# Performance work log

Hardware: AMD Instinct MI355X
Metric: run time of the kernel (lower is better)

Reference implementation:

```python
import jax, jax.numpy as jnp
import numpy as np

N = 100000      # nodes
E = 1200000     # edges (avg degree 12)
IN, H, OUT = 128, 64, 47
NUM_CONVS = 4   # num_layers=3 hidden SAGEConvs + 1 output SAGEConv


def setup_inputs() -> dict:
    key = jax.random.key(0)
    ks = jax.random.split(key, 2 + 1 + 2 * NUM_CONVS)
    x = jax.random.normal(ks[0], (N, IN), dtype=jnp.float32)
    edge_index = jax.random.randint(ks[1], (2, E), 0, N, dtype=jnp.int32)

    def lin(k, out_d, in_d):
        return jax.random.normal(k, (out_d, in_d), dtype=jnp.float32) / np.float32(np.sqrt(in_d))

    inp = {"x": x, "edge_index": edge_index}
    inp["W_in"] = lin(ks[2], H, IN)
    inp["b_in"] = jnp.zeros((H,), jnp.float32)
    dims = [(H, H), (H, H), (H, H), (OUT, H)]
    for i, (o, d) in enumerate(dims):
        inp[f"Wl{i}"] = lin(ks[3 + 2 * i], o, d)   # lin_l: applied to mean-aggregated neighbors (has bias)
        inp[f"Wr{i}"] = lin(ks[4 + 2 * i], o, d)   # lin_r: applied to root/self features (no bias)
        inp[f"bl{i}"] = jnp.zeros((o,), jnp.float32)
    return inp


def _sage_conv(x, src, dst, deg_inv, Wl, bl, Wr):
    # PyG SAGEConv (mean aggr): out_i = Wl @ mean_{j->i} x_j + bl + Wr @ x_i
    msg = x[src]                                               # [E, d] gather
    agg = jax.ops.segment_sum(msg, dst, num_segments=N)        # [N, d] scatter-add
    agg = agg * deg_inv[:, None]                               # mean
    return agg @ Wl.T + bl + x @ Wr.T


def reference(x, edge_index, W_in, b_in,
              Wl0, Wr0, bl0, Wl1, Wr1, bl1, Wl2, Wr2, bl2, Wl3, Wr3, bl3):
    src, dst = edge_index[0], edge_index[1]
    deg = jax.ops.segment_sum(jnp.ones((E,), x.dtype), dst, num_segments=N)
    deg_inv = jnp.where(deg > 0, 1.0 / jnp.maximum(deg, 1.0), 0.0)

    x = x @ W_in.T + b_in                                      # inProj
    inp = x
    x = jax.nn.relu(x)

    layers = [(Wl0, bl0, Wr0), (Wl1, bl1, Wr1), (Wl2, bl2, Wr2), (Wl3, bl3, Wr3)]
    for i, (Wl, bl, Wr) in enumerate(layers):
        x = _sage_conv(x, src, dst, deg_inv, Wl, bl, Wr)
        if i != NUM_CONVS - 1:
            x = jax.nn.relu(x)
            # dropout is identity in eval mode (training=False)
            x = x + 0.2 * inp
    return jax.nn.log_softmax(x, axis=-1)
```

## Files before the change

### kernel.cpp

```cpp
#include <hip/hip_runtime.h>
#include <hip/hip_fp16.h>

#define NN 100000
#define NE 1200000
#define DIN 128
#define DH 64
#define DOUT_FINAL 47
#define NPB 4
#define NBKT 391
#define EB 4096

typedef _Float16 half8 __attribute__((ext_vector_type(8)));
typedef float floatx4 __attribute__((ext_vector_type(4)));


__global__ void bucket_hist_k(const int* __restrict__ dst, int* __restrict__ bktCnt) {
    __shared__ int h[NBKT];
    int tid = threadIdx.x;
    for (int i = tid; i < NBKT; i += 256) h[i] = 0;
    __syncthreads();
    for (int e = blockIdx.x * 256 + tid; e < NE; e += gridDim.x * 256)
        atomicAdd(&h[dst[e] >> 8], 1);
    __syncthreads();
    for (int i = tid; i < NBKT; i += 256)
        if (h[i]) atomicAdd(&bktCnt[i], h[i]);
}

__global__ void bscan_k(const int* __restrict__ bktCnt, int* __restrict__ bktPtr) {
    __shared__ int s[512];
    int tid = threadIdx.x;
    int v = (tid < NBKT) ? bktCnt[tid] : 0;
    s[tid] = v;
    __syncthreads();
    for (int off = 1; off < 512; off <<= 1) {
        int t = (tid >= off) ? s[tid - off] : 0;
        __syncthreads();
        s[tid] += t;
        __syncthreads();
    }
    if (tid < NBKT) bktPtr[tid] = s[tid] - v;
    if (tid == 0) bktPtr[NBKT] = NE;
}

__global__ void scatter_pairs_k(const int* __restrict__ src, const int* __restrict__ dst,
                                const int* __restrict__ bktPtr, int* __restrict__ bktCur,
                                int2* __restrict__ pairs) {
    __shared__ int h[NBKT];
    __shared__ int base[NBKT];
    __shared__ int cur[NBKT];
    int tid = threadIdx.x;
    int e0 = blockIdx.x * EB;
    int e1 = e0 + EB < NE ? e0 + EB : NE;
    for (int i = tid; i < NBKT; i += 256) { h[i] = 0; cur[i] = 0; }
    __syncthreads();
    for (int e = e0 + tid; e < e1; e += 256)
        atomicAdd(&h[dst[e] >> 8], 1);
    __syncthreads();
    for (int i = tid; i < NBKT; i += 256) {
        int c = h[i];
        base[i] = bktPtr[i] + (c ? atomicAdd(&bktCur[i], c) : 0);
    }
    __syncthreads();
    for (int e = e0 + tid; e < e1; e += 256) {
        int d = dst[e];
        int b = d >> 8;
        int p = base[b] + atomicAdd(&cur[b], 1);
        pairs[p] = make_int2(src[e], d);
    }
}

__global__ void count_node_k(const int2* __restrict__ pairs, const int* __restrict__ bktPtr,
                             int* __restrict__ cnt) {
    __shared__ int h[256];
    int tid = threadIdx.x;
    int b = blockIdx.x;
    h[tid] = 0;
    __syncthreads();
    int e1 = bktPtr[b + 1];
    for (int e = bktPtr[b] + tid; e < e1; e += 256)
        atomicAdd(&h[pairs[e].y & 255], 1);
    __syncthreads();
    int node = (b << 8) + tid;
    if (node < NN) cnt[node] = h[tid];
}

__global__ void scan1_k(const int* __restrict__ cnt, int* __restrict__ ptr,
                        int* __restrict__ bsum, float* __restrict__ dinv) {
    __shared__ int s[256];
    int tid = threadIdx.x;
    int i = blockIdx.x * 256 + tid;
    int v = (i < NN) ? cnt[i] : 0;
    s[tid] = v;
    __syncthreads();
    for (int off = 1; off < 256; off <<= 1) {
        int t = (tid >= off) ? s[tid - off] : 0;
        __syncthreads();
        s[tid] += t;
        __syncthreads();
    }
    if (i < NN) {
        ptr[i] = s[tid] - v;
        dinv[i] = (v > 0) ? 1.0f / (float)v : 0.0f;
    }
    if (tid == 255) bsum[blockIdx.x] = s[255];
}

__global__ void scan2_k(int* __restrict__ bsum, int nb) {
    __shared__ int s[512];
    int tid = threadIdx.x;
    int v = (tid < nb) ? bsum[tid] : 0;
    s[tid] = v;
    __syncthreads();
    for (int off = 1; off < 512; off <<= 1) {
        int t = (tid >= off) ? s[tid - off] : 0;
        __syncthreads();
        s[tid] += t;
        __syncthreads();
    }
    if (tid < nb) bsum[tid] = s[tid] - v;
}

__global__ void scan3_k(int* __restrict__ ptr, const int* __restrict__ bsum) {
    int i = blockIdx.x * 256 + threadIdx.x;
    if (i < NN) ptr[i] += bsum[blockIdx.x];
    if (i == 0) ptr[NN] = NE;
}

__global__ void fill_bucket_k(const int2* __restrict__ pairs, const int* __restrict__ bktPtr,
                              const int* __restrict__ ptr, int* __restrict__ csrc) {
    __shared__ int cur[256];
    __shared__ int sptr[256];
    int tid = threadIdx.x;
    int b = blockIdx.x;
    cur[tid] = 0;
    int node = (b << 8) + tid;
    sptr[tid] = (node < NN) ? ptr[node] : 0;
    __syncthreads();
    int e1 = bktPtr[b + 1];
    for (int e = bktPtr[b] + tid; e < e1; e += 256) {
        int2 pr = pairs[e];
        int lo = pr.y & 255;
        int r = atomicAdd(&cur[lo], 1);
        csrc[sptr[lo] + r] = pr.x;
    }
}


__global__ void convert_x_k(const float* __restrict__ x, __half* __restrict__ xh) {
    int i = (blockIdx.x * 256 + threadIdx.x) * 8;
    if (i >= NN * DIN) return;
    float4 v0 = *(const float4*)&x[i];
    float4 v1 = *(const float4*)&x[i + 4];
    union { __half h[8]; uint4 u; } pk;
    pk.h[0] = __float2half(v0.x); pk.h[1] = __float2half(v0.y);
    pk.h[2] = __float2half(v0.z); pk.h[3] = __float2half(v0.w);
    pk.h[4] = __float2half(v1.x); pk.h[5] = __float2half(v1.y);
    pk.h[6] = __float2half(v1.z); pk.h[7] = __float2half(v1.w);
    *(uint4*)&xh[i] = pk.u;
}

__global__ void convert_w_k(const float* __restrict__ Win,
                            const float* __restrict__ Wl0, const float* __restrict__ Wr0,
                            const float* __restrict__ Wl1, const float* __restrict__ Wr1,
                            const float* __restrict__ Wl2, const float* __restrict__ Wr2,
                            const float* __restrict__ Wl3, const float* __restrict__ Wr3,
                            __half* __restrict__ wh) {
    int id = blockIdx.x * 256 + threadIdx.x;
    if (id >= 8192 + 8 * 4096) return;
    float v;
    if (id < 8192) {
        v = Win[id];
    } else {
        int q = id - 8192;
        int mi = q >> 12;
        int local = q & 4095;
        int r = local >> 6, c = local & 63;
        const float* srcs[8] = {Wl0, Wr0, Wl1, Wr1, Wl2, Wr2, Wl3, Wr3};
        int dout = (mi >= 6) ? DOUT_FINAL : 64;
        v = (r < dout) ? srcs[mi][r * 64 + c] : 0.0f;
    }
    wh[id] = __float2half(v);
}


__global__ __launch_bounds__(256) void gemm_in_mfma(const _Float16* __restrict__ Xh,
                                                    const _Float16* __restrict__ Wh,
                                                    const float* __restrict__ bias,
                                                    __half* __restrict__ hinph,
                                                    __half* __restrict__ xah) {
    int wave = threadIdx.x >> 6, lane = threadIdx.x & 63;
    int lr = lane & 15, kg = lane >> 4;
    int m0 = blockIdx.x * 128 + wave * 32;
    floatx4 acc[2][4];
    #pragma unroll
    for (int mt = 0; mt < 2; ++mt)
        #pragma unroll
        for (int nt = 0; nt < 4; ++nt) acc[mt][nt] = (floatx4){0.f, 0.f, 0.f, 0.f};
    half8 az = {};
    #pragma unroll
    for (int kc = 0; kc < 4; ++kc) {
        half8 a[2];
        #pragma unroll
        for (int mt = 0; mt < 2; ++mt) {
            int m = m0 + mt * 16 + lr;
            a[mt] = (m < NN) ? *(const half8*)&Xh[(size_t)m * 128 + kc * 32 + kg * 8] : az;
        }
        #pragma unroll
        for (int nt = 0; nt < 4; ++nt) {
            half8 b = *(const half8*)&Wh[(size_t)(nt * 16 + lr) * 128 + kc * 32 + kg * 8];
            #pragma unroll
            for (int mt = 0; mt < 2; ++mt)
                acc[mt][nt] = __builtin_amdgcn_mfma_f32_16x16x32_f16(a[mt], b, acc[mt][nt], 0, 0, 0);
        }
    }
    #pragma unroll
    for (int mt = 0; mt < 2; ++mt)
        #pragma unroll
        for (int nt = 0; nt < 4; ++nt) {
            int n = nt * 16 + lr;
            float bv = bias[n];
            #pragma unroll
            for (int j = 0; j < 4; ++j) {
                int m = m0 + mt * 16 + kg * 4 + j;
                if (m < NN) {
                    float v = acc[mt][nt][j] + bv;
                    hinph[(size_t)m * 64 + n] = __float2half(v);
                    xah[(size_t)m * 64 + n] = __float2half(fmaxf(v, 0.0f));
                }
            }
        }
}

__global__ __launch_bounds__(256) void gemm_dual_mfma(const _Float16* __restrict__ Xh,
                                                      const _Float16* __restrict__ Wlh,
                                                      const _Float16* __restrict__ Wrh,
                                                      __half* __restrict__ ylh,
                                                      __half* __restrict__ yrh) {
    int wave = threadIdx.x >> 6, lane = threadIdx.x & 63;
    int lr = lane & 15, kg = lane >> 4;
    int m0 = blockIdx.x * 128 + wave * 32;
    floatx4 accL[2][4], accR[2][4];
    #pragma unroll
    for (int mt = 0; mt < 2; ++mt)
        #pragma unroll
        for (int nt = 0; nt < 4; ++nt) {
            accL[mt][nt] = (floatx4){0.f, 0.f, 0.f, 0.f};
            accR[mt][nt] = (floatx4){0.f, 0.f, 0.f, 0.f};
        }
    half8 az = {};
    #pragma unroll
    for (int kc = 0; kc < 2; ++kc) {
        half8 a[2];
        #pragma unroll
        for (int mt = 0; mt < 2; ++mt) {
            int m = m0 + mt * 16 + lr;
            a[mt] = (m < NN) ? *(const half8*)&Xh[(size_t)m * 64 + kc * 32 + kg * 8] : az;
        }
        #pragma unroll
        for (int nt = 0; nt < 4; ++nt) {
            half8 bl = *(const half8*)&Wlh[(size_t)(nt * 16 + lr) * 64 + kc * 32 + kg * 8];
            half8 br = *(const half8*)&Wrh[(size_t)(nt * 16 + lr) * 64 + kc * 32 + kg * 8];
            #pragma unroll
            for (int mt = 0; mt < 2; ++mt) {
                accL[mt][nt] = __builtin_amdgcn_mfma_f32_16x16x32_f16(a[mt], bl, accL[mt][nt], 0, 0, 0);
                accR[mt][nt] = __builtin_amdgcn_mfma_f32_16x16x32_f16(a[mt], br, accR[mt][nt], 0, 0, 0);
            }
        }
    }
    #pragma unroll
    for (int mt = 0; mt < 2; ++mt)
        #pragma unroll
        for (int nt = 0; nt < 4; ++nt) {
            int n = nt * 16 + lr;
            #pragma unroll
            for (int j = 0; j < 4; ++j) {
                int m = m0 + mt * 16 + kg * 4 + j;
                if (m < NN) {
                    ylh[(size_t)m * 64 + n] = __float2half(accL[mt][nt][j]);
                    yrh[(size_t)m * 64 + n] = __float2half(accR[mt][nt][j]);
                }
            }
        }
}


__device__ __forceinline__ float2 gather_sum2(const __half* __restrict__ ylh,
                                              const int* __restrict__ csrc,
                                              int eb, int ee, int lane) {
    int half = lane >> 5;
    int fo = (lane & 31) * 4;
    const char* base = (const char*)ylh;
    float accx = 0.0f, accy = 0.0f;
    for (int e0 = eb; e0 < ee; e0 += 64) {
        int rem = ee - e0;
        int m = rem < 64 ? rem : 64;
        int sv = (lane < m) ? csrc[e0 + lane] : 0;
        int j = 0;
        for (; j + 8 <= m; j += 8) {
            int sA = __shfl(sv, j + 0 + half);
            int sB = __shfl(sv, j + 2 + half);
            int sC = __shfl(sv, j + 4 + half);
            int sD = __shfl(sv, j + 6 + half);
            float2 a = __half22float2(*(const __half2*)(base + (sA * 128 + fo)));
            float2 b = __half22float2(*(const __half2*)(base + (sB * 128 + fo)));
            float2 c = __half22float2(*(const __half2*)(base + (sC * 128 + fo)));
            float2 d = __half22float2(*(const __half2*)(base + (sD * 128 + fo)));
            accx += (a.x + b.x) + (c.x + d.x);
            accy += (a.y + b.y) + (c.y + d.y);
        }
        for (; j + 2 <= m; j += 2) {
            int s = __shfl(sv, j + half);
            float2 a = __half22float2(*(const __half2*)(base + (s * 128 + fo)));
            accx += a.x;
            accy += a.y;
        }
        if (j < m) {
            int s = __shfl(sv, j);
            if (half == 0) {
                float2 a = __half22float2(*(const __half2*)(base + (s * 128 + fo)));
                accx += a.x;
                accy += a.y;
            }
        }
    }
    accx += __shfl_xor(accx, 32);
    accy += __shfl_xor(accy, 32);
    return make_float2(accx, accy);
}


__global__ void aggregate_mid_k(const __half* __restrict__ ylh, const __half* __restrict__ yrh,
                                const __half* __restrict__ hinph,
                                const int* __restrict__ ptr, const int* __restrict__ csrc,
                                const float* __restrict__ dinv, const float* __restrict__ bl,
                                __half* __restrict__ outp) {
    int tid = threadIdx.x;
    int w = tid >> 6, lane = tid & 63;
    int i = blockIdx.x * NPB + w;
    if (i >= NN) return;
    float2 acc = gather_sum2(ylh, csrc, ptr[i], ptr[i + 1], lane);
    int half = lane >> 5;
    int f0 = (lane & 31) * 2;
    float dv = dinv[i];
    float2 yrv = __half22float2(*(const __half2*)&yrh[(size_t)i * 64 + f0]);
    float2 blv = *(const float2*)&bl[f0];
    float2 hv = __half22float2(*(const __half2*)&hinph[(size_t)i * 64 + f0]);
    float rx = fmaxf(acc.x * dv + yrv.x + blv.x, 0.0f) + 0.2f * hv.x;
    float ry = fmaxf(acc.y * dv + yrv.y + blv.y, 0.0f) + 0.2f * hv.y;
    if (half == 0) {
        __half2 hv2;
        hv2.x = __float2half(rx);
        hv2.y = __float2half(ry);
        *(__half2*)&outp[(size_t)i * 64 + f0] = hv2;
    }
}


__global__ void aggregate_final_k(const __half* __restrict__ ylh, const __half* __restrict__ yrh,
                                  const int* __restrict__ ptr, const int* __restrict__ csrc,
                                  const float* __restrict__ dinv, const float* __restrict__ bl,
                                  float* __restrict__ outp) {
    int tid = threadIdx.x;
    int w = tid >> 6, lane = tid & 63;
    int i = blockIdx.x * NPB + w;
    if (i >= NN) return;
    float2 acc = gather_sum2(ylh, csrc, ptr[i], ptr[i + 1], lane);
    int half = lane >> 5;
    int f0 = (lane & 31) * 2;
    float dv = dinv[i];
    float2 yrv = __half22float2(*(const __half2*)&yrh[(size_t)i * 64 + f0]);
    float b0 = (f0 < DOUT_FINAL) ? bl[f0] : 0.0f;
    float b1 = (f0 + 1 < DOUT_FINAL) ? bl[f0 + 1] : 0.0f;
    float vx = (f0 < DOUT_FINAL) ? acc.x * dv + yrv.x + b0 : -__builtin_inff();
    float vy = (f0 + 1 < DOUT_FINAL) ? acc.y * dv + yrv.y + b1 : -__builtin_inff();
    float mx = fmaxf(vx, vy);
    for (int o = 16; o; o >>= 1) mx = fmaxf(mx, __shfl_xor(mx, o));
    float ex = ((f0 < DOUT_FINAL) ? expf(vx - mx) : 0.0f) +
               ((f0 + 1 < DOUT_FINAL) ? expf(vy - mx) : 0.0f);
    float s = ex;
    for (int o = 16; o; o >>= 1) s += __shfl_xor(s, o);
    float ls = logf(s);
    if (half == 0) {
        if (f0 < DOUT_FINAL)     outp[(size_t)i * DOUT_FINAL + f0] = vx - mx - ls;
        if (f0 + 1 < DOUT_FINAL) outp[(size_t)i * DOUT_FINAL + f0 + 1] = vy - mx - ls;
    }
}


extern "C" void kernel_launch(void* const* d_in, const int* in_sizes, int n_in,
                              void* d_out, int out_size, void* d_ws, size_t ws_size,
                              hipStream_t stream) {
    const float* x    = (const float*)d_in[0];
    const int*   ei   = (const int*)d_in[1];
    const float* Win  = (const float*)d_in[2];
    const float* bin  = (const float*)d_in[3];
    const float* Wl0  = (const float*)d_in[4];
    const float* Wr0  = (const float*)d_in[5];
    const float* bl0  = (const float*)d_in[6];
    const float* Wl1  = (const float*)d_in[7];
    const float* Wr1  = (const float*)d_in[8];
    const float* bl1  = (const float*)d_in[9];
    const float* Wl2  = (const float*)d_in[10];
    const float* Wr2  = (const float*)d_in[11];
    const float* bl2  = (const float*)d_in[12];
    const float* Wl3  = (const float*)d_in[13];
    const float* Wr3  = (const float*)d_in[14];
    const float* bl3  = (const float*)d_in[15];
    float* out = (float*)d_out;

    const int* src = ei;
    const int* dst = ei + NE;

    size_t off = 0;
    auto alloc = [&](size_t bytes) -> void* {
        void* p = (char*)d_ws + off;
        off += (bytes + 255) & ~(size_t)255;
        return p;
    };
    int*    bkt    = (int*)alloc((size_t)2 * NBKT * 4);
    int*    bktPtr = (int*)alloc((size_t)(NBKT + 1) * 4);
    int2*   pairs  = (int2*)alloc((size_t)NE * 8);
    int*    cnt    = (int*)alloc((size_t)NN * 4);
    int*    ptr    = (int*)alloc((size_t)(NN + 1) * 4);
    float*  dinv   = (float*)alloc((size_t)NN * 4);
    int*    csrc   = (int*)alloc((size_t)NE * 4);
    int*    bsum   = (int*)alloc(512 * 4);
    __half* xh     = (__half*)alloc((size_t)NN * 128 * 2);
    __half* wh     = (__half*)alloc((size_t)(8192 + 8 * 4096) * 2);
    __half* hinph  = (__half*)alloc((size_t)NN * 64 * 2);
    __half* xah    = (__half*)alloc((size_t)NN * 64 * 2);
    __half* xbh    = (__half*)alloc((size_t)NN * 64 * 2);
    __half* ylh    = (__half*)alloc((size_t)NN * 64 * 2);
    __half* yrh    = (__half*)alloc((size_t)NN * 64 * 2);
    int*    bktCnt = bkt;
    int*    bktCur = bkt + NBKT;

    __half* Winh = wh;
    __half* Wl0h = wh + 8192;
    __half* Wr0h = Wl0h + 4096;
    __half* Wl1h = Wr0h + 4096;
    __half* Wr1h = Wl1h + 4096;
    __half* Wl2h = Wr1h + 4096;
    __half* Wr2h = Wl2h + 4096;
    __half* Wl3h = Wr2h + 4096;
    __half* Wr3h = Wl3h + 4096;

    const int NB_NODE = (NN + 255) / 256;
    const int NB_AGG  = (NN + NPB - 1) / NPB;
    const int NB_GEMM = (NN + 127) / 128;
    const int NB_SCAT = (NE + EB - 1) / EB;
    const int NB_XC   = (NN * DIN / 8 + 255) / 256;
    const int NB_WC   = (8192 + 8 * 4096 + 255) / 256;

    convert_x_k<<<NB_XC, 256, 0, stream>>>(x, xh);
    convert_w_k<<<NB_WC, 256, 0, stream>>>(Win, Wl0, Wr0, Wl1, Wr1, Wl2, Wr2, Wl3, Wr3, wh);

    hipMemsetAsync(bkt, 0, (size_t)2 * NBKT * 4, stream);
    bucket_hist_k<<<512, 256, 0, stream>>>(dst, bktCnt);
    bscan_k<<<1, 512, 0, stream>>>(bktCnt, bktPtr);
    scatter_pairs_k<<<NB_SCAT, 256, 0, stream>>>(src, dst, bktPtr, bktCur, pairs);
    count_node_k<<<NBKT, 256, 0, stream>>>(pairs, bktPtr, cnt);
    scan1_k<<<NB_NODE, 256, 0, stream>>>(cnt, ptr, bsum, dinv);
    scan2_k<<<1, 512, 0, stream>>>(bsum, NB_NODE);
    scan3_k<<<NB_NODE, 256, 0, stream>>>(ptr, bsum);
    fill_bucket_k<<<NBKT, 256, 0, stream>>>(pairs, bktPtr, ptr, csrc);

    gemm_in_mfma<<<NB_GEMM, 256, 0, stream>>>((const _Float16*)xh, (const _Float16*)Winh, bin, hinph, xah);

    gemm_dual_mfma<<<NB_GEMM, 256, 0, stream>>>((const _Float16*)xah, (const _Float16*)Wl0h, (const _Float16*)Wr0h, ylh, yrh);
    aggregate_mid_k<<<NB_AGG, 256, 0, stream>>>(ylh, yrh, hinph, ptr, csrc, dinv, bl0, xbh);
    gemm_dual_mfma<<<NB_GEMM, 256, 0, stream>>>((const _Float16*)xbh, (const _Float16*)Wl1h, (const _Float16*)Wr1h, ylh, yrh);
    aggregate_mid_k<<<NB_AGG, 256, 0, stream>>>(ylh, yrh, hinph, ptr, csrc, dinv, bl1, xah);
    gemm_dual_mfma<<<NB_GEMM, 256, 0, stream>>>((const _Float16*)xah, (const _Float16*)Wl2h, (const _Float16*)Wr2h, ylh, yrh);
    aggregate_mid_k<<<NB_AGG, 256, 0, stream>>>(ylh, yrh, hinph, ptr, csrc, dinv, bl2, xbh);
    gemm_dual_mfma<<<NB_GEMM, 256, 0, stream>>>((const _Float16*)xbh, (const _Float16*)Wl3h, (const _Float16*)Wr3h, ylh, yrh);
    aggregate_final_k<<<NB_AGG, 256, 0, stream>>>(ylh, yrh, ptr, csrc, dinv, bl3, out);
}
```

Measured before the change: 343.7 us.

## Interleave gathers for four nodes per wavefront in aggregation kernels

Each wavefront now aggregates four destination nodes instead of one. The gather loops for the four nodes are interleaved so more independent memory loads are in flight per wave, which is meant to hide gather latency and cut per-wave setup overhead. Blocks now cover 16 nodes, so there are fewer blocks. The risks are load imbalance when the four degrees differ, extra control flow and register use, and lower occupancy.

```diff
diff --git a/kernel.cpp b/kernel.cpp
--- a/kernel.cpp
+++ b/kernel.cpp
@@ -6,7 +6,7 @@
 #define DIN 128
 #define DH 64
 #define DOUT_FINAL 47
-#define NPB 4
+#define NPB4 16
 #define NBKT 391
 #define EB 4096
 
@@ -284,48 +284,85 @@
 }
 
 
-__device__ __forceinline__ float2 gather_sum2(const __half* __restrict__ ylh,
-                                              const int* __restrict__ csrc,
-                                              int eb, int ee, int lane) {
+#define GQ_BODY8(sv, j, ax, ay)                                                   \
+    {                                                                             \
+        int sA = __shfl(sv, j + 0 + half);                                        \
+        int sB = __shfl(sv, j + 2 + half);                                        \
+        int sC = __shfl(sv, j + 4 + half);                                        \
+        int sD = __shfl(sv, j + 6 + half);                                        \
+        float2 a = __half22float2(*(const __half2*)(base + (sA * 128 + fo)));     \
+        float2 b = __half22float2(*(const __half2*)(base + (sB * 128 + fo)));     \
+        float2 c = __half22float2(*(const __half2*)(base + (sC * 128 + fo)));     \
+        float2 d = __half22float2(*(const __half2*)(base + (sD * 128 + fo)));     \
+        ax += (a.x + b.x) + (c.x + d.x);                                          \
+        ay += (a.y + b.y) + (c.y + d.y);                                          \
+    }
+#define GQ_BODY2(sv, j, ax, ay)                                                   \
+    {                                                                             \
+        int s = __shfl(sv, j + half);                                             \
+        float2 a = __half22float2(*(const __half2*)(base + (s * 128 + fo)));      \
+        ax += a.x; ay += a.y;                                                     \
+    }
+#define GQ_BODY1(sv, j, ax, ay)                                                   \
+    {                                                                             \
+        int s = __shfl(sv, j);                                                    \
+        if (half == 0) {                                                          \
+            float2 a = __half22float2(*(const __half2*)(base + (s * 128 + fo)));  \
+            ax += a.x; ay += a.y;                                                 \
+        }                                                                         \
+    }
+
+__device__ __forceinline__ void gather_quad(const __half* __restrict__ ylh,
+                                            const int* __restrict__ csrc,
+                                            int eb0, int ee0, int eb1, int ee1,
+                                            int eb2, int ee2, int eb3, int ee3,
+                                            int lane,
+                                            float2& r0, float2& r1, float2& r2, float2& r3) {
     int half = lane >> 5;
     int fo = (lane & 31) * 4;
     const char* base = (const char*)ylh;
-    float accx = 0.0f, accy = 0.0f;
-    for (int e0 = eb; e0 < ee; e0 += 64) {
-        int rem = ee - e0;
-        int m = rem < 64 ? rem : 64;
-        int sv = (lane < m) ? csrc[e0 + lane] : 0;
-        int j = 0;
-        for (; j + 8 <= m; j += 8) {
-            int sA = __shfl(sv, j + 0 + half);
-            int sB = __shfl(sv, j + 2 + half);
-            int sC = __shfl(sv, j + 4 + half);
-            int sD = __shfl(sv, j + 6 + half);
-            float2 a = __half22float2(*(const __half2*)(base + (sA * 128 + fo)));
-            float2 b = __half22float2(*(const __half2*)(base + (sB * 128 + fo)));
-            float2 c = __half22float2(*(const __half2*)(base + (sC * 128 + fo)));
-            float2 d = __half22float2(*(const __half2*)(base + (sD * 128 + fo)));
-            accx += (a.x + b.x) + (c.x + d.x);
-            accy += (a.y + b.y) + (c.y + d.y);
-        }
-        for (; j + 2 <= m; j += 2) {
-            int s = __shfl(sv, j + half);
-            float2 a = __half22float2(*(const __half2*)(base + (s * 128 + fo)));
-            accx += a.x;
-            accy += a.y;
-        }
-        if (j < m) {
-            int s = __shfl(sv, j);
-            if (half == 0) {
-                float2 a = __half22float2(*(const __half2*)(base + (s * 128 + fo)));
-                accx += a.x;
-                accy += a.y;
-            }
-        }
-    }
-    accx += __shfl_xor(accx, 32);
-    accy += __shfl_xor(accy, 32);
-    return make_float2(accx, accy);
+    float a0x = 0.f, a0y = 0.f, a1x = 0.f, a1y = 0.f;
+    float a2x = 0.f, a2y = 0.f, a3x = 0.f, a3y = 0.f;
+
+    int e0 = eb0, e1 = eb1, e2 = eb2, e3 = eb3;
+    while (e0 < ee0 || e1 < ee1 || e2 < ee2 || e3 < ee3) {
+        int m0 = 0, m1 = 0, m2 = 0, m3 = 0;
+        int sv0 = 0, sv1 = 0, sv2 = 0, sv3 = 0;
+        if (e0 < ee0) { int r = ee0 - e0; m0 = r < 64 ? r : 64; sv0 = (lane < m0) ? csrc[e0 + lane] : 0; }
+        if (e1 < ee1) { int r = ee1 - e1; m1 = r < 64 ? r : 64; sv1 = (lane < m1) ? csrc[e1 + lane] : 0; }
+        if (e2 < ee2) { int r = ee2 - e2; m2 = r < 64 ? r : 64; sv2 = (lane < m2) ? csrc[e2 + lane] : 0; }
+        if (e3 < ee3) { int r = ee3 - e3; m3 = r < 64 ? r : 64; sv3 = (lane < m3) ? csrc[e3 + lane] : 0; }
+        int j0 = 0, j1 = 0, j2 = 0, j3 = 0;
+        bool more = true;
+        while (more) {
+            more = false;
+            if (j0 + 8 <= m0) { GQ_BODY8(sv0, j0, a0x, a0y); j0 += 8; more = true; }
+            if (j1 + 8 <= m1) { GQ_BODY8(sv1, j1, a1x, a1y); j1 += 8; more = true; }
+            if (j2 + 8 <= m2) { GQ_BODY8(sv2, j2, a2x, a2y); j2 += 8; more = true; }
+            if (j3 + 8 <= m3) { GQ_BODY8(sv3, j3, a3x, a3y); j3 += 8; more = true; }
+        }
+        more = true;
+        while (more) {
+            more = false;
+            if (j0 + 2 <= m0) { GQ_BODY2(sv0, j0, a0x, a0y); j0 += 2; more = true; }
+            if (j1 + 2 <= m1) { GQ_BODY2(sv1, j1, a1x, a1y); j1 += 2; more = true; }
+            if (j2 + 2 <= m2) { GQ_BODY2(sv2, j2, a2x, a2y); j2 += 2; more = true; }
+            if (j3 + 2 <= m3) { GQ_BODY2(sv3, j3, a3x, a3y); j3 += 2; more = true; }
+        }
+        if (j0 < m0) GQ_BODY1(sv0, j0, a0x, a0y);
+        if (j1 < m1) GQ_BODY1(sv1, j1, a1x, a1y);
+        if (j2 < m2) GQ_BODY1(sv2, j2, a2x, a2y);
+        if (j3 < m3) GQ_BODY1(sv3, j3, a3x, a3y);
+        e0 += 64; e1 += 64; e2 += 64; e3 += 64;
+    }
+    a0x += __shfl_xor(a0x, 32); a0y += __shfl_xor(a0y, 32);
+    a1x += __shfl_xor(a1x, 32); a1y += __shfl_xor(a1y, 32);
+    a2x += __shfl_xor(a2x, 32); a2y += __shfl_xor(a2y, 32);
+    a3x += __shfl_xor(a3x, 32); a3y += __shfl_xor(a3y, 32);
+    r0 = make_float2(a0x, a0y);
+    r1 = make_float2(a1x, a1y);
+    r2 = make_float2(a2x, a2y);
+    r3 = make_float2(a3x, a3y);
 }
 
 
@@ -336,21 +373,34 @@
                                 __half* __restrict__ outp) {
     int tid = threadIdx.x;
     int w = tid >> 6, lane = tid & 63;
-    int i = blockIdx.x * NPB + w;
-    if (i >= NN) return;
-    float2 acc = gather_sum2(ylh, csrc, ptr[i], ptr[i + 1], lane);
+    int ib = blockIdx.x * NPB4 + w * 4;
+    if (ib >= NN) return;
+    int eb[4], ee[4];
+    #pragma unroll
+    for (int n = 0; n < 4; ++n) {
+        int i = ib + n;
+        if (i < NN) { eb[n] = ptr[i]; ee[n] = ptr[i + 1]; }
+        else        { eb[n] = 0; ee[n] = 0; }
+    }
+    float2 acc0, acc1, acc2, acc3;
+    gather_quad(ylh, csrc, eb[0], ee[0], eb[1], ee[1], eb[2], ee[2], eb[3], ee[3],
+                lane, acc0, acc1, acc2, acc3);
+
     int half = lane >> 5;
     int f0 = (lane & 31) * 2;
-    float dv = dinv[i];
-    float2 yrv = __half22float2(*(const __half2*)&yrh[(size_t)i * 64 + f0]);
+    if (half != 0) return;
     float2 blv = *(const float2*)&bl[f0];
-    float2 hv = __half22float2(*(const __half2*)&hinph[(size_t)i * 64 + f0]);
-    float rx = fmaxf(acc.x * dv + yrv.x + blv.x, 0.0f) + 0.2f * hv.x;
-    float ry = fmaxf(acc.y * dv + yrv.y + blv.y, 0.0f) + 0.2f * hv.y;
-    if (half == 0) {
+    float2 accs[4] = {acc0, acc1, acc2, acc3};
+    #pragma unroll
+    for (int n = 0; n < 4; ++n) {
+        int i = ib + n;
+        if (i >= NN) continue;
+        float dv = dinv[i];
+        float2 yrv = __half22float2(*(const __half2*)&yrh[(size_t)i * 64 + f0]);
+        float2 hv = __half22float2(*(const __half2*)&hinph[(size_t)i * 64 + f0]);
         __half2 hv2;
-        hv2.x = __float2half(rx);
-        hv2.y = __float2half(ry);
+        hv2.x = __float2half(fmaxf(accs[n].x * dv + yrv.x + blv.x, 0.0f) + 0.2f * hv.x);
+        hv2.y = __float2half(fmaxf(accs[n].y * dv + yrv.y + blv.y, 0.0f) + 0.2f * hv.y);
         *(__half2*)&outp[(size_t)i * 64 + f0] = hv2;
     }
 }
@@ -362,27 +412,43 @@
                                   float* __restrict__ outp) {
     int tid = threadIdx.x;
     int w = tid >> 6, lane = tid & 63;
-    int i = blockIdx.x * NPB + w;
-    if (i >= NN) return;
-    float2 acc = gather_sum2(ylh, csrc, ptr[i], ptr[i + 1], lane);
+    int ib = blockIdx.x * NPB4 + w * 4;
+    if (ib >= NN) return;
+    int eb[4], ee[4];
+    #pragma unroll
+    for (int n = 0; n < 4; ++n) {
+        int i = ib + n;
+        if (i < NN) { eb[n] = ptr[i]; ee[n] = ptr[i + 1]; }
+        else        { eb[n] = 0; ee[n] = 0; }
+    }
+    float2 acc0, acc1, acc2, acc3;
+    gather_quad(ylh, csrc, eb[0], ee[0], eb[1], ee[1], eb[2], ee[2], eb[3], ee[3],
+                lane, acc0, acc1, acc2, acc3);
+
     int half = lane >> 5;
     int f0 = (lane & 31) * 2;
-    float dv = dinv[i];
-    float2 yrv = __half22float2(*(const __half2*)&yrh[(size_t)i * 64 + f0]);
     float b0 = (f0 < DOUT_FINAL) ? bl[f0] : 0.0f;
     float b1 = (f0 + 1 < DOUT_FINAL) ? bl[f0 + 1] : 0.0f;
-    float vx = (f0 < DOUT_FINAL) ? acc.x * dv + yrv.x + b0 : -__builtin_inff();
-    float vy = (f0 + 1 < DOUT_FINAL) ? acc.y * dv + yrv.y + b1 : -__builtin_inff();
-    float mx = fmaxf(vx, vy);
-    for (int o = 16; o; o >>= 1) mx = fmaxf(mx, __shfl_xor(mx, o));
-    float ex = ((f0 < DOUT_FINAL) ? expf(vx - mx) : 0.0f) +
-               ((f0 + 1 < DOUT_FINAL) ? expf(vy - mx) : 0.0f);
-    float s = ex;
-    for (int o = 16; o; o >>= 1) s += __shfl_xor(s, o);
-    float ls = logf(s);
-    if (half == 0) {
-        if (f0 < DOUT_FINAL)     outp[(size_t)i * DOUT_FINAL + f0] = vx - mx - ls;
-        if (f0 + 1 < DOUT_FINAL) outp[(size_t)i * DOUT_FINAL + f0 + 1] = vy - mx - ls;
+    float2 accs[4] = {acc0, acc1, acc2, acc3};
+    #pragma unroll
+    for (int n = 0; n < 4; ++n) {
+        int i = ib + n;
+        if (i >= NN) continue;
+        float dv = dinv[i];
+        float2 yrv = __half22float2(*(const __half2*)&yrh[(size_t)i * 64 + f0]);
+        float vx = (f0 < DOUT_FINAL) ? accs[n].x * dv + yrv.x + b0 : -__builtin_inff();
+        float vy = (f0 + 1 < DOUT_FINAL) ? accs[n].y * dv + yrv.y + b1 : -__builtin_inff();
+        float mx = fmaxf(vx, vy);
+        for (int o = 16; o; o >>= 1) mx = fmaxf(mx, __shfl_xor(mx, o));
+        float ex = ((f0 < DOUT_FINAL) ? expf(vx - mx) : 0.0f) +
+                   ((f0 + 1 < DOUT_FINAL) ? expf(vy - mx) : 0.0f);
+        float s = ex;
+        for (int o = 16; o; o >>= 1) s += __shfl_xor(s, o);
+        float ls = logf(s);
+        if (half == 0) {
+            if (f0 < DOUT_FINAL)     outp[(size_t)i * DOUT_FINAL + f0] = vx - mx - ls;
+            if (f0 + 1 < DOUT_FINAL) outp[(size_t)i * DOUT_FINAL + f0 + 1] = vy - mx - ls;
+        }
     }
 }
 
@@ -446,7 +512,7 @@
     __half* Wr3h = Wl3h + 4096;
 
     const int NB_NODE = (NN + 255) / 256;
-    const int NB_AGG  = (NN + NPB - 1) / NPB;
+    const int NB_AGG  = (NN + NPB4 - 1) / NPB4;
     const int NB_GEMM = (NN + 127) / 128;
     const int NB_SCAT = (NE + EB - 1) / EB;
     const int NB_XC   = (NN * DIN / 8 + 255) / 256;
```

Result: no change. 337.4 us (-1.8%).
